# Performance work log

Hardware: AMD Instinct MI355X
Metric: run time of the kernel (lower is better)

The kernel has to match this reference:

```python
import jax, jax.numpy as jnp
import numpy as np
from jax import lax

B, T, L, D, K, VOCAB = 64, 128, 32, 128, 64, 50000


def setup_inputs() -> dict:
    key = jax.random.key(0)
    ks = jax.random.split(key, 8)
    prgrph = jax.random.randint(ks[0], (B, T, L), 0, VOCAB, dtype=jnp.int32)
    prgrph_mask = jax.random.randint(ks[1], (B, T, L), 0, 2, dtype=jnp.int32).astype(bool)
    embedding_matrix = jax.random.normal(ks[2], (VOCAB, D), dtype=jnp.float32)
    positional_mask = jax.random.normal(ks[3], (L, D), dtype=jnp.float32)
    Uw = jax.random.normal(ks[4], (D, D), dtype=jnp.float32) * 0.05
    Vw = jax.random.normal(ks[5], (D, D), dtype=jnp.float32) * 0.05
    Ww = jax.random.normal(ks[6], (D, D), dtype=jnp.float32) * 0.05
    keys = jax.random.normal(ks[7], (B, K, D), dtype=jnp.float32)
    return {"prgrph": prgrph, "prgrph_mask": prgrph_mask,
            "embedding_matrix": embedding_matrix, "positional_mask": positional_mask,
            "Uw": Uw, "Vw": Vw, "Ww": Ww, "keys": keys}


def _entity_scan(enc, sent_mask, keys, Uw, Vw, Ww):
    # enc: [B,T,D] encoded sentences; sent_mask: [B,T] bool; keys: [B,K,D]
    h0 = jnp.zeros_like(keys)  # initial entity hidden state = zeros

    def step(h, xs):
        s, m = xs  # s: [B,D], m: [B]
        # Eq 2: gate = sigmoid(s . h + s . k)  -> [B,K]
        g = jax.nn.sigmoid(jnp.einsum('bkd,bd->bk', h + keys, s))
        # Eq 3: h_tilda = sigmoid(h U + k V + s W)  -> [B,K,D]
        h_tilda = jax.nn.sigmoid(
            jnp.einsum('bkd,de->bke', h, Uw)
            + jnp.einsum('bkd,de->bke', keys, Vw)
            + (s @ Ww)[:, None, :])
        # Eq 4-5: add gated update, L2-normalize over embedding dim
        hn = h + g[..., None] * h_tilda
        hn = hn / jnp.sqrt(jnp.maximum(jnp.sum(hn * hn, axis=-1, keepdims=True), 1e-12))
        # only paragraphs with an active sentence at this step are updated
        h = jnp.where(m[:, None, None], hn, h)
        return h, None

    h_last, _ = lax.scan(step, h0, (jnp.swapaxes(enc, 0, 1), sent_mask.T))
    return h_last


def reference(prgrph, prgrph_mask, embedding_matrix, positional_mask, Uw, Vw, Ww, keys):
    # embed words; padded words contribute zero to the sentence encoding
    emb = embedding_matrix[prgrph] * prgrph_mask[..., None].astype(embedding_matrix.dtype)  # [B,T,L,D]
    # Sent_encoder: weighted bag of words with learned positional mask
    enc = jnp.einsum('btld,ld->btd', emb, positional_mask)  # [B,T,D]
    sent_mask = jnp.any(prgrph_mask, axis=2)  # [B,T]
    return _entity_scan(enc, sent_mask, keys, Uw, Vw, Ww)  # [B,K,D]
```

## Files before the change

kernel.cpp:

```cpp
#include <hip/hip_runtime.h>
#include <hip/hip_bf16.h>
#include <stdint.h>

#define B_ 64
#define T_ 128
#define L_ 32
#define D_ 128
#define K_ 64

#define FLAG_OFF 0
#define SM_OFF   256
#define ENC_OFF  (SM_OFF + B_*T_)
#define SW_OFF   (ENC_OFF + B_*T_*D_)
#define KS_OFF   (SW_OFF + B_*T_*D_)
#define KV_OFF   (KS_OFF + B_*T_*K_)

typedef __attribute__((ext_vector_type(8))) short short8b;
typedef __attribute__((ext_vector_type(4))) float f32x4;

union frag_cast { uint4 u; short8b s; };

__device__ __forceinline__ float sigmoidf_(float x){ return 1.0f/(1.0f + __expf(-x)); }

__device__ __forceinline__ unsigned short bfb(float x){
  __hip_bfloat16 h = __float2bfloat16(x);
  return __builtin_bit_cast(unsigned short, h);
}
__device__ __forceinline__ float bf2f(unsigned short u){
  return __uint_as_float(((unsigned)u) << 16);
}

__global__ __launch_bounds__(256) void k_detect(const uint8_t* __restrict__ m,
                                                int* __restrict__ flags){
  const unsigned* w = (const unsigned*)m;
  const int base = blockIdx.x * 512;
  unsigned acc = 0;
  acc |= w[base + threadIdx.x]       & 0xFFFFFF00u;
  acc |= w[base + threadIdx.x + 256] & 0xFFFFFF00u;
  int any = __syncthreads_or((int)(acc != 0u));
  if(threadIdx.x == 0) flags[blockIdx.x] = any;
}

__global__ __launch_bounds__(128) void k_enc(const int* __restrict__ prg,
                                             const uint8_t* __restrict__ pm8,
                                             const float* __restrict__ emb,
                                             const float* __restrict__ pos,
                                             const float* __restrict__ Ww,
                                             const float* __restrict__ keys,
                                             float* __restrict__ W){
  const int bt = blockIdx.x;
  const int b  = bt / T_;
  const int d  = threadIdx.x;
  int myf  = ((const int*)W)[FLAG_OFF + (d & 127)];
  int flag = __syncthreads_or(myf);
  __shared__ float keysl[K_*129];
  __shared__ float encl[D_];
  for(int r=0;r<K_;r++) keysl[r*129 + d] = keys[(b*K_ + r)*D_ + d];
  const int* pmi = (const int*)pm8;
  float acc = 0.f; int anym = 0;
  for(int l=0;l<L_;l++){
    int off = bt*L_ + l;
    int m = flag ? (int)pm8[off] : pmi[off];
    if(m){
      anym = 1;
      int idx = prg[off];
      acc += emb[idx*D_ + d] * pos[l*D_ + d];
    }
  }
  encl[d] = acc;
  W[ENC_OFF + bt*D_ + d] = acc;
  __syncthreads();
  float sw = 0.f;
  for(int e=0;e<D_;e++) sw += encl[e] * Ww[e*D_ + d];
  W[SW_OFF + bt*D_ + d] = sw;
  if(d < K_){
    float ks = 0.f;
    for(int dd=0;dd<D_;dd++) ks += keysl[d*129 + dd] * encl[dd];
    W[KS_OFF + bt*K_ + d] = ks;
  }
  if(d==0) W[SM_OFF + bt] = anym ? 1.f : 0.f;
}

__global__ __launch_bounds__(128) void k_kv(const float* __restrict__ keys,
                                            const float* __restrict__ Vw,
                                            float* __restrict__ W){
  const int bk = blockIdx.x;
  const int d  = threadIdx.x;
  __shared__ float kr[D_];
  kr[d] = keys[bk*D_ + d];
  __syncthreads();
  float acc = 0.f;
  for(int e=0;e<D_;e++) acc += kr[e] * Vw[e*D_ + d];
  W[KV_OFF + bk*D_ + d] = acc;
}

__global__ __attribute__((amdgpu_flat_work_group_size(64,64), amdgpu_waves_per_eu(1)))
void k_scan(const float* __restrict__ W,
            const float* __restrict__ Uw,
            float* __restrict__ out){
  const int b    = blockIdx.x >> 2;
  const int kg   = blockIdx.x & 3;
  const int lane = threadIdx.x;
  const int e    = lane & 15;
  const int q    = lane >> 4;

  __shared__ float ring [8*256];
  __shared__ float ringk[8*20];

  short8b ufrag[8][4];
  #pragma unroll
  for(int rt=0; rt<8; ++rt){
    #pragma unroll
    for(int kc=0; kc<4; ++kc){
      const float* r0 = &Uw[(32*kc + 4*q)*D_ + 16*rt + e];
      short8b f;
      #pragma unroll
      for(int j=0;j<8;++j) f[j] = (short)bfb(r0[((j>>2)*16 + (j&3))*D_]);
      ufrag[rt][kc] = f;
    }
  }
  f32x4 kvv[8];
  {
    const float* kvp = &W[KV_OFF + (b*K_ + kg*16 + e)*D_ + 4*q];
    #pragma unroll
    for(int rt=0;rt<8;++rt) kvv[rt] = *(const f32x4*)&kvp[16*rt];
  }
  f32x4 vY[8];
  #pragma unroll
  for(int rt=0;rt<8;++rt) vY[rt] = 0.f;

  const float* ENC = &W[ENC_OFF + b*T_*D_];
  const float* SWg = &W[SW_OFF  + b*T_*D_];
  const float* KSg = &W[KS_OFF  + b*T_*K_];
  const float* SM  = &W[SM_OFF  + b*T_];

  auto issue = [&](int t, f32x4& g, float& k, float& m){
    int tL = (t < T_) ? t : (T_-1);
    const float* src = (lane < 32) ? &ENC[tL*D_ + lane*4]
                                   : &SWg[tL*D_ + (lane-32)*4];
    g = *(const f32x4*)src;
    k = KSg[tL*K_ + kg*16 + e];
    m = SM[tL];
  };
  auto commit = [&](int t, const f32x4& g, float k, float m){
    int slot = t & 7;
    *(f32x4*)&ring[slot*256 + lane*4] = g;
    if(lane < 16)   ringk[slot*20 + lane] = k;
    if(lane == 16)  ringk[slot*20 + 16]   = m;
  };

  auto dostep = [&](int t, float sm){
    if(sm != 0.f){
      int slot = t & 7;
      f32x4 sv[8], sw[8];
      #pragma unroll
      for(int rt=0;rt<8;++rt){
        sv[rt] = *(const f32x4*)&ring[slot*256 +       16*rt + 4*q];
        sw[rt] = *(const f32x4*)&ring[slot*256 + 128 + 16*rt + 4*q];
      }
      float ks = ringk[slot*20 + e];

      short8b bhi[4], blo[4];
      #pragma unroll
      for(int kc=0;kc<4;++kc){
        const f32x4& va = vY[2*kc];
        const f32x4& vb = vY[2*kc+1];
        unsigned short a0=bfb(va[0]), a1=bfb(va[1]), a2=bfb(va[2]), a3=bfb(va[3]);
        unsigned short b0=bfb(vb[0]), b1=bfb(vb[1]), b2=bfb(vb[2]), b3=bfb(vb[3]);
        frag_cast fh;
        fh.u = make_uint4(((unsigned)a1<<16)|a0, ((unsigned)a3<<16)|a2,
                          ((unsigned)b1<<16)|b0, ((unsigned)b3<<16)|b2);
        unsigned short c0=bfb(va[0]-bf2f(a0)), c1=bfb(va[1]-bf2f(a1));
        unsigned short c2=bfb(va[2]-bf2f(a2)), c3=bfb(va[3]-bf2f(a3));
        unsigned short d0=bfb(vb[0]-bf2f(b0)), d1=bfb(vb[1]-bf2f(b1));
        unsigned short d2=bfb(vb[2]-bf2f(b2)), d3=bfb(vb[3]-bf2f(b3));
        frag_cast fl;
        fl.u = make_uint4(((unsigned)c1<<16)|c0, ((unsigned)c3<<16)|c2,
                          ((unsigned)d1<<16)|d0, ((unsigned)d3<<16)|d2);
        bhi[kc] = fh.s;
        blo[kc] = fl.s;
      }

      float n0=0.f,n1=0.f,n2=0.f,n3=0.f, g0=0.f,g1=0.f,g2=0.f,g3=0.f;
      #pragma unroll
      for(int rt=0;rt<8;++rt){
        n0 += vY[rt][0]*vY[rt][0];  g0 += vY[rt][0]*sv[rt][0];
        n1 += vY[rt][1]*vY[rt][1];  g1 += vY[rt][1]*sv[rt][1];
        n2 += vY[rt][2]*vY[rt][2];  g2 += vY[rt][2]*sv[rt][2];
        n3 += vY[rt][3]*vY[rt][3];  g3 += vY[rt][3]*sv[rt][3];
      }
      float ns = (n0+n1)+(n2+n3);
      float gs = (g0+g1)+(g2+g3);
      ns += __shfl_xor(ns,16);
      ns += __shfl_xor(ns,32);
      gs += __shfl_xor(gs,16);
      gs += __shfl_xor(gs,32);
      float n = rsqrtf(fmaxf(ns, 1e-12f));
      float g = sigmoidf_(fmaf(n, gs, ks));

      f32x4 ah[8], al[8];
      #pragma unroll
      for(int rt=0;rt<8;++rt){ ah[rt] = 0.f; al[rt] = 0.f; }
      #pragma unroll
      for(int rt=0;rt<8;++rt){
        #pragma unroll
        for(int kc=0;kc<4;++kc){
          ah[rt] = __builtin_amdgcn_mfma_f32_16x16x32_bf16(ufrag[rt][kc], bhi[kc], ah[rt], 0,0,0);
          al[rt] = __builtin_amdgcn_mfma_f32_16x16x32_bf16(ufrag[rt][kc], blo[kc], al[rt], 0,0,0);
        }
      }

      #pragma unroll
      for(int rt=0;rt<8;++rt){
        #pragma unroll
        for(int r=0;r<4;++r){
          float t0 = sw[rt][r] + kvv[rt][r];
          float x  = fmaf(n, ah[rt][r], fmaf(n, al[rt][r], t0));
          float ht = sigmoidf_(x);
          vY[rt][r] = fmaf(g, ht, n*vY[rt][r]);
        }
      }
    }
  };

  f32x4 gT; float kT, mT;
  #pragma unroll 1
  for(int s=0; s<7; ++s){ issue(s, gT, kT, mT); commit(s, gT, kT, mT); }
  f32x4 gP; float kP, mP;
  issue(7, gP, kP, mP);
  float smC = ringk[0*20 + 16];

  #pragma unroll 1
  for(int t=0; t<T_; ++t){
    commit(t+7, gP, kP, mP);
    issue (t+8, gP, kP, mP);
    float smN = ringk[((t+1)&7)*20 + 16];
    dostep(t, smC);
    smC = smN;
  }

  float ns = 0.f;
  #pragma unroll
  for(int rt=0;rt<8;++rt){
    #pragma unroll
    for(int r=0;r<4;++r) ns += vY[rt][r]*vY[rt][r];
  }
  ns += __shfl_xor(ns,16);
  ns += __shfl_xor(ns,32);
  float n = rsqrtf(fmaxf(ns, 1e-12f));
  float* op = &out[(b*K_ + kg*16 + e)*D_ + 4*q];
  #pragma unroll
  for(int rt=0;rt<8;++rt){
    f32x4 o;
    #pragma unroll
    for(int r=0;r<4;++r) o[r] = vY[rt][r]*n;
    *(f32x4*)&op[16*rt] = o;
  }
}

extern "C" void kernel_launch(void* const* d_in, const int* in_sizes, int n_in,
                              void* d_out, int out_size, void* d_ws, size_t ws_size,
                              hipStream_t stream) {
  const int*     prg  = (const int*)d_in[0];
  const uint8_t* pm   = (const uint8_t*)d_in[1];
  const float*   emb  = (const float*)d_in[2];
  const float*   pos  = (const float*)d_in[3];
  const float*   Uw   = (const float*)d_in[4];
  const float*   Vw   = (const float*)d_in[5];
  const float*   Ww   = (const float*)d_in[6];
  const float*   keys = (const float*)d_in[7];
  float* W   = (float*)d_ws;
  float* out = (float*)d_out;

  hipLaunchKernelGGL(k_detect, dim3(128),    dim3(256), 0, stream, pm, (int*)d_ws + FLAG_OFF);
  hipLaunchKernelGGL(k_enc,    dim3(B_*T_),  dim3(128), 0, stream, prg, pm, emb, pos, Ww, keys, W);
  hipLaunchKernelGGL(k_kv,     dim3(B_*K_),  dim3(128), 0, stream, keys, Vw, W);
  hipLaunchKernelGGL(k_scan,   dim3(B_*4),   dim3(64),  0, stream, W, Uw, out);
}
```

Measured before the change: 499.4 us.

## Stream scan inputs directly into LDS with global_load_lds and interleaved layout

Interleaves enc and s·W per timestep into one 256-float row and reorders the key-score buffer per key group, so the scan kernel can use direct global-to-LDS loads. The scan now preloads all key scores and sentence masks into LDS up front and keeps a 7-deep ring of enc/sW rows using vmcnt waits instead of register staging plus LDS stores. The mask-conditional branch becomes a select, so every step does the full compute. It depends on manual waitcnt correctness and drops the skip for inactive steps.

```diff
diff --git a/kernel.cpp b/kernel.cpp
--- a/kernel.cpp
+++ b/kernel.cpp
@@ -8,12 +8,11 @@
 #define D_ 128
 #define K_ 64
 
-#define FLAG_OFF 0
-#define SM_OFF   256
-#define ENC_OFF  (SM_OFF + B_*T_)
-#define SW_OFF   (ENC_OFF + B_*T_*D_)
-#define KS_OFF   (SW_OFF + B_*T_*D_)
-#define KV_OFF   (KS_OFF + B_*T_*K_)
+#define FLAG_OFF  0
+#define SM_OFF    256
+#define ENCSW_OFF (SM_OFF + B_*T_)
+#define KS2_OFF   (ENCSW_OFF + B_*T_*256)
+#define KV_OFF    (KS2_OFF + B_*4*T_*16)
 
 typedef __attribute__((ext_vector_type(8))) short short8b;
 typedef __attribute__((ext_vector_type(4))) float f32x4;
@@ -28,6 +27,15 @@
 }
 __device__ __forceinline__ float bf2f(unsigned short u){
   return __uint_as_float(((unsigned)u) << 16);
+}
+
+__device__ __forceinline__ void gl16(const float* g, float* l){
+  __builtin_amdgcn_global_load_lds((const __attribute__((address_space(1))) void*)g,
+                                   (__attribute__((address_space(3))) void*)l, 16, 0, 0);
+}
+__device__ __forceinline__ void gl4(const float* g, float* l){
+  __builtin_amdgcn_global_load_lds((const __attribute__((address_space(1))) void*)g,
+                                   (__attribute__((address_space(3))) void*)l, 4, 0, 0);
 }
 
 __global__ __launch_bounds__(256) void k_detect(const uint8_t* __restrict__ m,
@@ -50,6 +58,7 @@
                                              float* __restrict__ W){
   const int bt = blockIdx.x;
   const int b  = bt / T_;
+  const int t  = bt % T_;
   const int d  = threadIdx.x;
   int myf  = ((const int*)W)[FLAG_OFF + (d & 127)];
   int flag = __syncthreads_or(myf);
@@ -68,15 +77,15 @@
     }
   }
   encl[d] = acc;
-  W[ENC_OFF + bt*D_ + d] = acc;
+  W[ENCSW_OFF + bt*256 + d] = acc;
   __syncthreads();
   float sw = 0.f;
   for(int e=0;e<D_;e++) sw += encl[e] * Ww[e*D_ + d];
-  W[SW_OFF + bt*D_ + d] = sw;
+  W[ENCSW_OFF + bt*256 + 128 + d] = sw;
   if(d < K_){
     float ks = 0.f;
     for(int dd=0;dd<D_;dd++) ks += keysl[d*129 + dd] * encl[dd];
-    W[KS_OFF + bt*K_ + d] = ks;
+    W[KS2_OFF + ((b*4 + (d>>4))*T_ + t)*16 + (d&15)] = ks;
   }
   if(d==0) W[SM_OFF + bt] = anym ? 1.f : 0.f;
 }
@@ -104,8 +113,9 @@
   const int e    = lane & 15;
   const int q    = lane >> 4;
 
-  __shared__ float ring [8*256];
-  __shared__ float ringk[8*20];
+  __shared__ float ring[8*256];
+  __shared__ float ksl[T_*16];
+  __shared__ float sml[T_];
 
   short8b ufrag[8][4];
   #pragma unroll
@@ -129,114 +139,99 @@
   #pragma unroll
   for(int rt=0;rt<8;++rt) vY[rt] = 0.f;
 
-  const float* ENC = &W[ENC_OFF + b*T_*D_];
-  const float* SWg = &W[SW_OFF  + b*T_*D_];
-  const float* KSg = &W[KS_OFF  + b*T_*K_];
-  const float* SM  = &W[SM_OFF  + b*T_];
-
-  auto issue = [&](int t, f32x4& g, float& k, float& m){
-    int tL = (t < T_) ? t : (T_-1);
-    const float* src = (lane < 32) ? &ENC[tL*D_ + lane*4]
-                                   : &SWg[tL*D_ + (lane-32)*4];
-    g = *(const f32x4*)src;
-    k = KSg[tL*K_ + kg*16 + e];
-    m = SM[tL];
-  };
-  auto commit = [&](int t, const f32x4& g, float k, float m){
+  const float* ENCSW = &W[ENCSW_OFF + b*T_*256];
+  const float* KS2   = &W[KS2_OFF + (b*4 + kg)*T_*16];
+  const float* SMg   = &W[SM_OFF + b*T_];
+
+  #pragma unroll
+  for(int i=0;i<8;++i) gl16(&KS2[i*256 + lane*4], &ksl[i*256]);
+  gl4(&SMg[lane],      &sml[0]);
+  gl4(&SMg[64 + lane], &sml[64]);
+  #pragma unroll
+  for(int s=0;s<7;++s) gl16(&ENCSW[s*256 + lane*4], &ring[s*256]);
+
+  auto dostep = [&](int t){
     int slot = t & 7;
-    *(f32x4*)&ring[slot*256 + lane*4] = g;
-    if(lane < 16)   ringk[slot*20 + lane] = k;
-    if(lane == 16)  ringk[slot*20 + 16]   = m;
-  };
-
-  auto dostep = [&](int t, float sm){
-    if(sm != 0.f){
-      int slot = t & 7;
-      f32x4 sv[8], sw[8];
-      #pragma unroll
-      for(int rt=0;rt<8;++rt){
-        sv[rt] = *(const f32x4*)&ring[slot*256 +       16*rt + 4*q];
-        sw[rt] = *(const f32x4*)&ring[slot*256 + 128 + 16*rt + 4*q];
-      }
-      float ks = ringk[slot*20 + e];
-
-      short8b bhi[4], blo[4];
+    f32x4 sv[8], sw[8];
+    #pragma unroll
+    for(int rt=0;rt<8;++rt){
+      sv[rt] = *(const f32x4*)&ring[slot*256 +       16*rt + 4*q];
+      sw[rt] = *(const f32x4*)&ring[slot*256 + 128 + 16*rt + 4*q];
+    }
+    float ks = ksl[t*16 + e];
+    float sm = sml[t];
+
+    short8b bhi[4], blo[4];
+    #pragma unroll
+    for(int kc=0;kc<4;++kc){
+      const f32x4& va = vY[2*kc];
+      const f32x4& vb = vY[2*kc+1];
+      unsigned short a0=bfb(va[0]), a1=bfb(va[1]), a2=bfb(va[2]), a3=bfb(va[3]);
+      unsigned short b0=bfb(vb[0]), b1=bfb(vb[1]), b2=bfb(vb[2]), b3=bfb(vb[3]);
+      frag_cast fh;
+      fh.u = make_uint4(((unsigned)a1<<16)|a0, ((unsigned)a3<<16)|a2,
+                        ((unsigned)b1<<16)|b0, ((unsigned)b3<<16)|b2);
+      unsigned short c0=bfb(va[0]-bf2f(a0)), c1=bfb(va[1]-bf2f(a1));
+      unsigned short c2=bfb(va[2]-bf2f(a2)), c3=bfb(va[3]-bf2f(a3));
+      unsigned short d0=bfb(vb[0]-bf2f(b0)), d1=bfb(vb[1]-bf2f(b1));
+      unsigned short d2=bfb(vb[2]-bf2f(b2)), d3=bfb(vb[3]-bf2f(b3));
+      frag_cast fl;
+      fl.u = make_uint4(((unsigned)c1<<16)|c0, ((unsigned)c3<<16)|c2,
+                        ((unsigned)d1<<16)|d0, ((unsigned)d3<<16)|d2);
+      bhi[kc] = fh.s;
+      blo[kc] = fl.s;
+    }
+
+    float n0=0.f,n1=0.f,n2=0.f,n3=0.f, g0=0.f,g1=0.f,g2=0.f,g3=0.f;
+    #pragma unroll
+    for(int rt=0;rt<8;++rt){
+      n0 += vY[rt][0]*vY[rt][0];  g0 += vY[rt][0]*sv[rt][0];
+      n1 += vY[rt][1]*vY[rt][1];  g1 += vY[rt][1]*sv[rt][1];
+      n2 += vY[rt][2]*vY[rt][2];  g2 += vY[rt][2]*sv[rt][2];
+      n3 += vY[rt][3]*vY[rt][3];  g3 += vY[rt][3]*sv[rt][3];
+    }
+    float ns = (n0+n1)+(n2+n3);
+    float gs = (g0+g1)+(g2+g3);
+    ns += __shfl_xor(ns,16);
+    ns += __shfl_xor(ns,32);
+    gs += __shfl_xor(gs,16);
+    gs += __shfl_xor(gs,32);
+    float n = rsqrtf(fmaxf(ns, 1e-12f));
+    float g = sigmoidf_(fmaf(n, gs, ks));
+
+    f32x4 ah[8], al[8];
+    #pragma unroll
+    for(int rt=0;rt<8;++rt){ ah[rt] = 0.f; al[rt] = 0.f; }
+    #pragma unroll
+    for(int rt=0;rt<8;++rt){
       #pragma unroll
       for(int kc=0;kc<4;++kc){
-        const f32x4& va = vY[2*kc];
-        const f32x4& vb = vY[2*kc+1];
-        unsigned short a0=bfb(va[0]), a1=bfb(va[1]), a2=bfb(va[2]), a3=bfb(va[3]);
-        unsigned short b0=bfb(vb[0]), b1=bfb(vb[1]), b2=bfb(vb[2]), b3=bfb(vb[3]);
-        frag_cast fh;
-        fh.u = make_uint4(((unsigned)a1<<16)|a0, ((unsigned)a3<<16)|a2,
-                          ((unsigned)b1<<16)|b0, ((unsigned)b3<<16)|b2);
-        unsigned short c0=bfb(va[0]-bf2f(a0)), c1=bfb(va[1]-bf2f(a1));
-        unsigned short c2=bfb(va[2]-bf2f(a2)), c3=bfb(va[3]-bf2f(a3));
-        unsigned short d0=bfb(vb[0]-bf2f(b0)), d1=bfb(vb[1]-bf2f(b1));
-        unsigned short d2=bfb(vb[2]-bf2f(b2)), d3=bfb(vb[3]-bf2f(b3));
-        frag_cast fl;
-        fl.u = make_uint4(((unsigned)c1<<16)|c0, ((unsigned)c3<<16)|c2,
-                          ((unsigned)d1<<16)|d0, ((unsigned)d3<<16)|d2);
-        bhi[kc] = fh.s;
-        blo[kc] = fl.s;
+        ah[rt] = __builtin_amdgcn_mfma_f32_16x16x32_bf16(ufrag[rt][kc], bhi[kc], ah[rt], 0,0,0);
+        al[rt] = __builtin_amdgcn_mfma_f32_16x16x32_bf16(ufrag[rt][kc], blo[kc], al[rt], 0,0,0);
       }
-
-      float n0=0.f,n1=0.f,n2=0.f,n3=0.f, g0=0.f,g1=0.f,g2=0.f,g3=0.f;
+    }
+
+    bool upd = (sm != 0.f);
+    #pragma unroll
+    for(int rt=0;rt<8;++rt){
       #pragma unroll
-      for(int rt=0;rt<8;++rt){
-        n0 += vY[rt][0]*vY[rt][0];  g0 += vY[rt][0]*sv[rt][0];
-        n1 += vY[rt][1]*vY[rt][1];  g1 += vY[rt][1]*sv[rt][1];
-        n2 += vY[rt][2]*vY[rt][2];  g2 += vY[rt][2]*sv[rt][2];
-        n3 += vY[rt][3]*vY[rt][3];  g3 += vY[rt][3]*sv[rt][3];
+      for(int r=0;r<4;++r){
+        float t0 = sw[rt][r] + kvv[rt][r];
+        float x  = fmaf(n, ah[rt][r], fmaf(n, al[rt][r], t0));
+        float ht = sigmoidf_(x);
+        float vn = fmaf(g, ht, n*vY[rt][r]);
+        vY[rt][r] = upd ? vn : vY[rt][r];
       }
-      float ns = (n0+n1)+(n2+n3);
-      float gs = (g0+g1)+(g2+g3);
-      ns += __shfl_xor(ns,16);
-      ns += __shfl_xor(ns,32);
-      gs += __shfl_xor(gs,16);
-      gs += __shfl_xor(gs,32);
-      float n = rsqrtf(fmaxf(ns, 1e-12f));
-      float g = sigmoidf_(fmaf(n, gs, ks));
-
-      f32x4 ah[8], al[8];
-      #pragma unroll
-      for(int rt=0;rt<8;++rt){ ah[rt] = 0.f; al[rt] = 0.f; }
-      #pragma unroll
-      for(int rt=0;rt<8;++rt){
-        #pragma unroll
-        for(int kc=0;kc<4;++kc){
-          ah[rt] = __builtin_amdgcn_mfma_f32_16x16x32_bf16(ufrag[rt][kc], bhi[kc], ah[rt], 0,0,0);
-          al[rt] = __builtin_amdgcn_mfma_f32_16x16x32_bf16(ufrag[rt][kc], blo[kc], al[rt], 0,0,0);
-        }
-      }
-
-      #pragma unroll
-      for(int rt=0;rt<8;++rt){
-        #pragma unroll
-        for(int r=0;r<4;++r){
-          float t0 = sw[rt][r] + kvv[rt][r];
-          float x  = fmaf(n, ah[rt][r], fmaf(n, al[rt][r], t0));
-          float ht = sigmoidf_(x);
-          vY[rt][r] = fmaf(g, ht, n*vY[rt][r]);
-        }
-      }
     }
   };
-
-  f32x4 gT; float kT, mT;
-  #pragma unroll 1
-  for(int s=0; s<7; ++s){ issue(s, gT, kT, mT); commit(s, gT, kT, mT); }
-  f32x4 gP; float kP, mP;
-  issue(7, gP, kP, mP);
-  float smC = ringk[0*20 + 16];
 
   #pragma unroll 1
   for(int t=0; t<T_; ++t){
-    commit(t+7, gP, kP, mP);
-    issue (t+8, gP, kP, mP);
-    float smN = ringk[((t+1)&7)*20 + 16];
-    dostep(t, smC);
-    smC = smN;
+    int r = t+7 < T_ ? t+7 : T_-1;
+    gl16(&ENCSW[r*256 + lane*4], &ring[((t+7)&7)*256]);
+    asm volatile("s_waitcnt vmcnt(7)" ::: "memory");
+    __builtin_amdgcn_sched_barrier(0);
+    dostep(t);
   }
 
   float ns = 0.f;
```

Measured after the change: 528.0 us. 5.7% more time.
